# Optimization experiments

Hardware: AMD Instinct MI355X
Metric: run time of the kernel (lower is better)

Reference implementation:

```python
import jax, jax.numpy as jnp
import numpy as np
from jax.scipy.linalg import expm

MS = 8  # matrix_size = sqrt(dims), dims=64


def setup_inputs() -> dict:
    key = jax.random.key(0)
    k1, k2, k3 = jax.random.split(key, 3)
    x = jax.random.normal(k1, (16384, MS), dtype=jnp.float32)
    t = jax.random.uniform(k2, (512,), dtype=jnp.float32)
    M = jax.random.normal(k3, (MS, MS), dtype=jnp.float32) * 0.01
    M0 = jnp.zeros((MS, MS), dtype=jnp.float32)
    return {"x": x, "t": t, "M": M, "M0": M0}


def reference(x, t, M, M0):
    # A = skew_symmetric(M + M0)
    B = M + M0
    A = (B - B.T) * 0.5                      # [MS, MS]
    tA = t[:, None, None] * A[None]          # [T, MS, MS]
    E = jax.vmap(expm)(tA)                   # [T, MS, MS] batched matrix exponential
    # out[t, n, i] = sum_j E[t, i, j] * x[n, j]
    out = jnp.einsum('tij,nj->tni', E, x)    # [T, N, MS]
    return out
```

## Files before the change

### kernel.cpp

```cpp
#include <hip/hip_runtime.h>

__global__ void expm_kernel(const float* __restrict__ M, const float* __restrict__ M0,
                            const float* __restrict__ t, float* __restrict__ E) {
    const int b = blockIdx.x;
    const int lane = threadIdx.x;
    const int i = lane >> 3;
    const int j = lane & 7;

    __shared__ float sA[64];
    __shared__ float sP[64];

    const float bij = M[i * 8 + j] + M0[i * 8 + j];
    const float bji = M[j * 8 + i] + M0[j * 8 + i];
    const float ta = t[b] * 0.5f * (bij - bji);

    sA[lane] = ta;
    float e = (i == j ? 1.0f : 0.0f) + ta;
    float p = ta;
    __syncthreads();

    for (int k = 2; k <= 12; ++k) {
        sP[lane] = p;
        __syncthreads();
        float s = 0.0f;
        #pragma unroll
        for (int l = 0; l < 8; ++l) {
            s = fmaf(sP[i * 8 + l], sA[l * 8 + j], s);
        }
        p = s * (1.0f / (float)k);
        e += p;
        __syncthreads();
    }

    E[b * 64 + lane] = e;
}

#define APPLY_G 8

__global__ __launch_bounds__(256) void apply_kernel(const float* __restrict__ Eall,
                                                    const float* __restrict__ x,
                                                    float* __restrict__ out,
                                                    int N) {
    const int t = blockIdx.y;

    __shared__ float sE[64];
    if (threadIdx.x < 64) sE[threadIdx.x] = Eall[t * 64 + threadIdx.x];
    __syncthreads();

    float e[64];
    #pragma unroll
    for (int c = 0; c < 64; ++c) e[c] = sE[c];

    const int n0 = blockIdx.x * (256 * APPLY_G) + threadIdx.x;
    const float4* __restrict__ x4 = (const float4*)x;
    float4* __restrict__ o4 = (float4*)(out + (size_t)t * (size_t)N * 8);

    #pragma unroll
    for (int g = 0; g < APPLY_G; ++g) {
        const int n = n0 + g * 256;
        if (n < N) {
            const float4 a = x4[2 * n];
            const float4 b = x4[2 * n + 1];
            const float xs[8] = {a.x, a.y, a.z, a.w, b.x, b.y, b.z, b.w};
            float y[8];
            #pragma unroll
            for (int ii = 0; ii < 8; ++ii) {
                float s = 0.0f;
                #pragma unroll
                for (int jj = 0; jj < 8; ++jj) {
                    s = fmaf(e[ii * 8 + jj], xs[jj], s);
                }
                y[ii] = s;
            }
            o4[2 * n]     = make_float4(y[0], y[1], y[2], y[3]);
            o4[2 * n + 1] = make_float4(y[4], y[5], y[6], y[7]);
        }
    }
}

extern "C" void kernel_launch(void* const* d_in, const int* in_sizes, int n_in,
                              void* d_out, int out_size, void* d_ws, size_t ws_size,
                              hipStream_t stream) {
    const float* x  = (const float*)d_in[0];
    const float* t  = (const float*)d_in[1];
    const float* M  = (const float*)d_in[2];
    const float* M0 = (const float*)d_in[3];
    float* out = (float*)d_out;
    float* E = (float*)d_ws;

    const int N = in_sizes[0] / 8;
    const int T = in_sizes[1];

    hipLaunchKernelGGL(expm_kernel, dim3(T), dim3(64), 0, stream, M, M0, t, E);

    const int gx = (N + 256 * APPLY_G - 1) / (256 * APPLY_G);
    hipLaunchKernelGGL(apply_kernel, dim3(gx, T), dim3(256), 0, stream, E, x, out, N);
}
```

Baseline: 267.4 us.

## Split output rows across thread pairs with coalesced nontemporal float4 stores

New measurement: 272.0 us. About the same (+1.7%).

```diff
diff --git a/kernel.cpp b/kernel.cpp
--- a/kernel.cpp
+++ b/kernel.cpp
@@ -1,4 +1,6 @@
 #include <hip/hip_runtime.h>
+
+typedef float vfloat4 __attribute__((ext_vector_type(4)));
 
 __global__ void expm_kernel(const float* __restrict__ M, const float* __restrict__ M0,
                             const float* __restrict__ t, float* __restrict__ E) {
@@ -42,38 +44,43 @@
                                                     float* __restrict__ out,
                                                     int N) {
     const int t = blockIdx.y;
+    const int tid = threadIdx.x;
+    const int h = tid & 1;
+    const int twoN = N * 2;
 
-    __shared__ float sE[64];
-    if (threadIdx.x < 64) sE[threadIdx.x] = Eall[t * 64 + threadIdx.x];
-    __syncthreads();
+    const float4* __restrict__ Ep = (const float4*)(Eall + t * 64 + h * 32);
+    float eh[32];
+    #pragma unroll
+    for (int q = 0; q < 8; ++q) {
+        const float4 v = Ep[q];
+        eh[q * 4 + 0] = v.x; eh[q * 4 + 1] = v.y;
+        eh[q * 4 + 2] = v.z; eh[q * 4 + 3] = v.w;
+    }
 
-    float e[64];
-    #pragma unroll
-    for (int c = 0; c < 64; ++c) e[c] = sE[c];
-
-    const int n0 = blockIdx.x * (256 * APPLY_G) + threadIdx.x;
+    const int k0 = blockIdx.x * (256 * APPLY_G) + tid;
     const float4* __restrict__ x4 = (const float4*)x;
-    float4* __restrict__ o4 = (float4*)(out + (size_t)t * (size_t)N * 8);
+    vfloat4* __restrict__ o4 = (vfloat4*)out + (size_t)t * (size_t)twoN;
 
     #pragma unroll
     for (int g = 0; g < APPLY_G; ++g) {
-        const int n = n0 + g * 256;
-        if (n < N) {
+        const int k = k0 + g * 256;
+        if (k < twoN) {
+            const int n = k >> 1;
             const float4 a = x4[2 * n];
             const float4 b = x4[2 * n + 1];
             const float xs[8] = {a.x, a.y, a.z, a.w, b.x, b.y, b.z, b.w};
-            float y[8];
+            float y[4];
             #pragma unroll
-            for (int ii = 0; ii < 8; ++ii) {
+            for (int r = 0; r < 4; ++r) {
                 float s = 0.0f;
                 #pragma unroll
                 for (int jj = 0; jj < 8; ++jj) {
-                    s = fmaf(e[ii * 8 + jj], xs[jj], s);
+                    s = fmaf(eh[r * 8 + jj], xs[jj], s);
                 }
-                y[ii] = s;
+                y[r] = s;
             }
-            o4[2 * n]     = make_float4(y[0], y[1], y[2], y[3]);
-            o4[2 * n + 1] = make_float4(y[4], y[5], y[6], y[7]);
+            vfloat4 v = {y[0], y[1], y[2], y[3]};
+            __builtin_nontemporal_store(v, &o4[k]);
         }
     }
 }
@@ -93,6 +100,6 @@
 
     hipLaunchKernelGGL(expm_kernel, dim3(T), dim3(64), 0, stream, M, M0, t, E);
 
-    const int gx = (N + 256 * APPLY_G - 1) / (256 * APPLY_G);
+    const int gx = (N * 2 + 256 * APPLY_G - 1) / (256 * APPLY_G);
     hipLaunchKernelGGL(apply_kernel, dim3(gx, T), dim3(256), 0, stream, E, x, out, N);
 }
```
